# Kernel tuning notes

Hardware: AMD Instinct MI355X
Metric: run time of the kernel (lower is better)

## Reference

```python
import jax, jax.numpy as jnp
import numpy as np

H, D = 24, 128
HID = H * D  # 3072
IP_DIM = 2048
B, S_IMG, S_TXT, L_IP = 1, 1024, 512, 16
EPS = 1e-6
IP_SCALE = 1.0


def _rms(x, w):
    v = jnp.mean(jnp.square(x), axis=-1, keepdims=True)
    return x * jax.lax.rsqrt(v + EPS) * w


def _heads(x):
    b, s, _ = x.shape
    return x.reshape(b, s, H, D).transpose(0, 2, 1, 3)  # [b,H,s,D]


def _unheads(x):
    b, h, s, d = x.shape
    return x.transpose(0, 2, 1, 3).reshape(b, s, h * d)


def _rope(x, cos, sin):
    # diffusers flux apply_rotary_emb (use_real, unbind_dim=-1): interleaved pairs
    xr = x.reshape(x.shape[:-1] + (D // 2, 2))
    xrot = jnp.stack([-xr[..., 1], xr[..., 0]], axis=-1).reshape(x.shape)
    return x * cos + xrot * sin


def _sdpa(q, k, v):
    scale = 1.0 / jnp.sqrt(jnp.asarray(D, q.dtype))
    s = jnp.einsum('bhqd,bhkd->bhqk', q, k) * scale
    return jnp.einsum('bhqk,bhkd->bhqd', jax.nn.softmax(s, axis=-1), v)


def setup_inputs() -> dict:
    ks = iter(jax.random.split(jax.random.key(0), 24))
    std = 0.02
    lin = lambda k, di, do: std * jax.random.normal(k, (di, do), jnp.float32)
    z = lambda: jnp.zeros((HID,), jnp.float32)
    ones = lambda: jnp.ones((D,), jnp.float32)
    return {
        'hidden_states': jax.random.normal(next(ks), (B, S_IMG, HID), jnp.float32),
        'encoder_hidden_states': jax.random.normal(next(ks), (B, S_TXT, HID), jnp.float32),
        'ip_hidden_states': jax.random.normal(next(ks), (B, L_IP, IP_DIM), jnp.float32),
        'rope_cos': jax.random.uniform(next(ks), (S_TXT + S_IMG, D), jnp.float32),
        'rope_sin': jax.random.uniform(next(ks), (S_TXT + S_IMG, D), jnp.float32),
        'Wq': lin(next(ks), HID, HID), 'bq': z(),
        'Wk': lin(next(ks), HID, HID), 'bk': z(),
        'Wv': lin(next(ks), HID, HID), 'bv': z(),
        'norm_q_w': ones(), 'norm_k_w': ones(),
        'Waq': lin(next(ks), HID, HID), 'baq': z(),
        'Wak': lin(next(ks), HID, HID), 'bak': z(),
        'Wav': lin(next(ks), HID, HID), 'bav': z(),
        'norm_added_q_w': ones(), 'norm_added_k_w': ones(),
        'Wo': lin(next(ks), HID, HID), 'bo': z(),
        'Wadd_out': lin(next(ks), HID, HID), 'badd_out': z(),
        'Wk_ip': lin(next(ks), IP_DIM, HID), 'bk_ip': z(),
        'Wv_ip': lin(next(ks), IP_DIM, HID), 'bv_ip': z(),
        'norm_ip_q_w': ones(), 'norm_ip_k_w': ones(),
    }


def reference(hidden_states, encoder_hidden_states, ip_hidden_states, rope_cos, rope_sin,
              Wq, bq, Wk, bk, Wv, bv, norm_q_w, norm_k_w,
              Waq, baq, Wak, bak, Wav, bav, norm_added_q_w, norm_added_k_w,
              Wo, bo, Wadd_out, badd_out,
              Wk_ip, bk_ip, Wv_ip, bv_ip, norm_ip_q_w, norm_ip_k_w):
    s_txt = encoder_hidden_states.shape[1]
    # image-token projections
    q = hidden_states @ Wq + bq
    k = hidden_states @ Wk + bk
    v = hidden_states @ Wv + bv

    # IP-adapter cross-attention branch (uses q pre-RMSNorm / pre-RoPE)
    ip_q = _rms(_heads(q), norm_ip_q_w)                               # [B,H,S_img,D]
    ip_k = _rms(_heads(ip_hidden_states @ Wk_ip + bk_ip), norm_ip_k_w)  # [B,H,L_ip,D]
    ip_v = _heads(ip_hidden_states @ Wv_ip + bv_ip)
    ip_out = _unheads(_sdpa(ip_q, ip_k, ip_v))                        # [B,S_img,HID]

    qh = _rms(_heads(q), norm_q_w)
    kh = _rms(_heads(k), norm_k_w)
    vh = _heads(v)

    # text-token (encoder) projections
    eq = _rms(_heads(encoder_hidden_states @ Waq + baq), norm_added_q_w)
    ek = _rms(_heads(encoder_hidden_states @ Wak + bak), norm_added_k_w)
    ev = _heads(encoder_hidden_states @ Wav + bav)

    qf = _rope(jnp.concatenate([eq, qh], axis=2), rope_cos, rope_sin)
    kf = _rope(jnp.concatenate([ek, kh], axis=2), rope_cos, rope_sin)
    vf = jnp.concatenate([ev, vh], axis=2)

    out = _unheads(_sdpa(qf, kf, vf))                                 # [B,S_txt+S_img,HID]
    enc_out, img_out = out[:, :s_txt], out[:, s_txt:]
    img_out = img_out + ip_out * IP_SCALE
    img_out = img_out @ Wo + bo
    enc_out = enc_out @ Wadd_out + badd_out
    return (img_out, enc_out)
```

## Files before the change

kernel.cpp:

```cpp
#include <hip/hip_runtime.h>

typedef __bf16 bf16x8 __attribute__((ext_vector_type(8)));
typedef float f32x4 __attribute__((ext_vector_type(4)));
typedef unsigned short u16;
typedef unsigned int u32;

#define QSCALE 0.08838834764831845f

static __device__ __forceinline__ float bf2f(u16 u) {
  union { float f; u32 i; } x; x.i = ((u32)u) << 16; return x.f;
}
static __device__ __forceinline__ u16 f2bf(float f) {
  union { float f; u32 i; } x; x.f = f;
  u32 r = x.i + 0x7fffu + ((x.i >> 16) & 1u);
  return (u16)(r >> 16);
}
static __device__ __forceinline__ void gload16(const void* gp, void* lp) {
  __builtin_amdgcn_global_load_lds(
      (const __attribute__((address_space(1))) u32*)gp,
      (__attribute__((address_space(3))) u32*)lp, 16, 0, 0);
}

__global__ __launch_bounds__(256) void k_conv_acts(
    const float* __restrict__ hs, const float* __restrict__ ehs, const float* __restrict__ iph,
    u16* __restrict__ hsb, u16* __restrict__ ehsb, u16* __restrict__ ipb)
{
  int i = blockIdx.x * 256 + threadIdx.x;
  const float* s; u16* d; int j;
  if (i < 786432)        { s = hs;  d = hsb;  j = i; }
  else if (i < 1179648)  { s = ehs; d = ehsb; j = i - 786432; }
  else                   { s = iph; d = ipb;  j = i - 1179648; }
  float4 v = ((const float4*)s)[j];
  uint2 o;
  o.x = (u32)f2bf(v.x) | ((u32)f2bf(v.y) << 16);
  o.y = (u32)f2bf(v.z) | ((u32)f2bf(v.w) << 16);
  ((uint2*)d)[j] = o;
}

struct WT { const float* src; u16* dst; int K; };
struct WTPack { WT w[10]; };

__global__ __launch_bounds__(256) void k_transp_w(WTPack p)
{
  WT d = p.w[blockIdx.z];
  int K = d.K;
  int k0 = blockIdx.y * 64;
  if (k0 >= K) return;
  int n0 = blockIdx.x * 64;
  __shared__ u16 T[64 * 72];
  int tid = threadIdx.x;
  #pragma unroll
  for (int i = 0; i < 4; i++) {
    int idx = tid + i * 256;
    int r = idx >> 4, ch = idx & 15;
    float4 v = *(const float4*)(d.src + (size_t)(k0 + r) * 3072 + n0 + ch * 4);
    T[(ch*4+0)*72 + r] = f2bf(v.x);
    T[(ch*4+1)*72 + r] = f2bf(v.y);
    T[(ch*4+2)*72 + r] = f2bf(v.z);
    T[(ch*4+3)*72 + r] = f2bf(v.w);
  }
  __syncthreads();
  #pragma unroll
  for (int i = 0; i < 2; i++) {
    int idx = tid + i * 256;
    int r = idx >> 3, ch = idx & 7;
    uint4 v = *(const uint4*)(T + r * 72 + ch * 8);
    *(uint4*)(d.dst + (size_t)(n0 + r) * K + k0 + ch * 8) = v;
  }
}

struct GJob { const u16* A; const u16* W; const float* bias; void* C; int M; int K; int blk0; int out_f32; };
struct GPack { GJob j[8]; int njobs; };

__global__ __launch_bounds__(256) void k_gemm(GPack p)
{
  __shared__ u16 As[128 * 32];
  __shared__ u16 Bs[128 * 32];
  int bid = blockIdx.x;
  int ji = 0;
  while (ji + 1 < p.njobs && bid >= p.j[ji+1].blk0) ji++;
  GJob J = p.j[ji];
  int local = bid - J.blk0;
  int m0 = (local / 24) * 128;
  int n0 = (local % 24) * 128;

  int tid = threadIdx.x, w = tid >> 6, lane = tid & 63, l15 = lane & 15, quad = lane >> 4;
  int wm = (w >> 1) * 64, wn = (w & 1) * 64;
  f32x4 acc[4][4] = {};

  int s0 = tid, s1 = tid + 256;
  const u16* Ag0 = J.A + (size_t)(m0 + (s0 >> 2)) * J.K + (s0 & 3) * 8;
  const u16* Ag1 = J.A + (size_t)(m0 + (s1 >> 2)) * J.K + (s1 & 3) * 8;
  const u16* Bg0 = J.W + (size_t)(n0 + (s0 >> 2)) * J.K + (s0 & 3) * 8;
  const u16* Bg1 = J.W + (size_t)(n0 + (s1 >> 2)) * J.K + (s1 & 3) * 8;
  u16* lA0 = As + w * 512;
  u16* lA1 = As + 2048 + w * 512;
  u16* lB0 = Bs + w * 512;
  u16* lB1 = Bs + 2048 + w * 512;

  for (int k0 = 0; k0 < J.K; k0 += 32) {
    gload16(Ag0 + k0, lA0);
    gload16(Ag1 + k0, lA1);
    gload16(Bg0 + k0, lB0);
    gload16(Bg1 + k0, lB1);
    __syncthreads();
    bf16x8 af[4], bfr[4];
    #pragma unroll
    for (int t = 0; t < 4; t++) {
      af[t]  = *(const bf16x8*)(As + (wm + t * 16 + l15) * 32 + quad * 8);
      bfr[t] = *(const bf16x8*)(Bs + (wn + t * 16 + l15) * 32 + quad * 8);
    }
    #pragma unroll
    for (int mt = 0; mt < 4; mt++)
      #pragma unroll
      for (int nt = 0; nt < 4; nt++)
        acc[mt][nt] = __builtin_amdgcn_mfma_f32_16x16x32_bf16(af[mt], bfr[nt], acc[mt][nt], 0, 0, 0);
    __syncthreads();
  }

  #pragma unroll
  for (int mt = 0; mt < 4; mt++) {
    int row = m0 + wm + mt * 16 + quad * 4;
    #pragma unroll
    for (int nt = 0; nt < 4; nt++) {
      int col = n0 + wn + nt * 16 + l15;
      float bv = J.bias[col];
      #pragma unroll
      for (int r = 0; r < 4; r++) {
        if (row + r < J.M) {
          float v = acc[mt][nt][r] + bv;
          if (J.out_f32) ((float*)J.C)[(size_t)(row + r) * 3072 + col] = v;
          else           ((u16*)J.C)[(size_t)(row + r) * 3072 + col] = f2bf(v);
        }
      }
    }
  }
}

__global__ __launch_bounds__(256) void k_pack_qk(
    const u16* __restrict__ q, const u16* __restrict__ k,
    const u16* __restrict__ eq, const u16* __restrict__ ek,
    const u16* __restrict__ ipk,
    const float* __restrict__ cosr, const float* __restrict__ sinr,
    const float* __restrict__ nq, const float* __restrict__ nk,
    const float* __restrict__ naq, const float* __restrict__ nak,
    const float* __restrict__ nipq, const float* __restrict__ nipk,
    u16* __restrict__ Qf, u16* __restrict__ Kf, u16* __restrict__ Qip, u16* __restrict__ Kip)
{
  int u = blockIdx.x * 4 + (threadIdx.x >> 6);
  int lane = threadIdx.x & 63;
  int d0 = lane * 2;
  if (u < 36864) {
    int t = u / 24, h = u % 24;
    bool txt = t < 512;
    const u16* qrow = txt ? eq + (size_t)t * 3072 : q + (size_t)(t - 512) * 3072;
    const u16* krow = txt ? ek + (size_t)t * 3072 : k + (size_t)(t - 512) * 3072;
    u32 qv = ((const u32*)(qrow + h * 128))[lane];
    u32 kv = ((const u32*)(krow + h * 128))[lane];
    float q0 = bf2f((u16)qv), q1 = bf2f((u16)(qv >> 16));
    float k0 = bf2f((u16)kv), k1 = bf2f((u16)(kv >> 16));
    float sq = q0 * q0 + q1 * q1, sk = k0 * k0 + k1 * k1;
    #pragma unroll
    for (int off = 32; off > 0; off >>= 1) {
      sq += __shfl_xor(sq, off, 64);
      sk += __shfl_xor(sk, off, 64);
    }
    float rq = rsqrtf(sq * (1.0f / 128.0f) + 1e-6f);
    float rk = rsqrtf(sk * (1.0f / 128.0f) + 1e-6f);
    const float* wq = txt ? naq : nq;
    const float* wk = txt ? nak : nk;
    float2 c = ((const float2*)(cosr + (size_t)t * 128))[lane];
    float2 s = ((const float2*)(sinr + (size_t)t * 128))[lane];
    float xq0 = q0 * rq * wq[d0] * QSCALE, xq1 = q1 * rq * wq[d0 + 1] * QSCALE;
    float xk0 = k0 * rk * wk[d0],          xk1 = k1 * rk * wk[d0 + 1];
    u32 oq = (u32)f2bf(xq0 * c.x - xq1 * s.x) | ((u32)f2bf(xq1 * c.y + xq0 * s.y) << 16);
    u32 ok = (u32)f2bf(xk0 * c.x - xk1 * s.x) | ((u32)f2bf(xk1 * c.y + xk0 * s.y) << 16);
    ((u32*)(Qf + ((size_t)h * 1536 + t) * 128))[lane] = oq;
    ((u32*)(Kf + ((size_t)h * 1536 + t) * 128))[lane] = ok;
    if (!txt) {
      float y0 = q0 * rq * nipq[d0] * QSCALE, y1 = q1 * rq * nipq[d0 + 1] * QSCALE;
      u32 oy = (u32)f2bf(y0) | ((u32)f2bf(y1) << 16);
      ((u32*)(Qip + ((size_t)h * 1024 + (t - 512)) * 128))[lane] = oy;
    }
  } else {
    int u2 = u - 36864;
    if (u2 < 384) {
      int h = u2 >> 4, t = u2 & 15;
      u32 v = ((const u32*)(ipk + (size_t)t * 3072 + h * 128))[lane];
      float x0 = bf2f((u16)v), x1 = bf2f((u16)(v >> 16));
      float ss = x0 * x0 + x1 * x1;
      #pragma unroll
      for (int off = 32; off > 0; off >>= 1) ss += __shfl_xor(ss, off, 64);
      float rr = rsqrtf(ss * (1.0f / 128.0f) + 1e-6f);
      u32 o = (u32)f2bf(x0 * rr * nipk[d0]) | ((u32)f2bf(x1 * rr * nipk[d0 + 1]) << 16);
      ((u32*)(Kip + ((size_t)h * 64 + t) * 128))[lane] = o;
    }
  }
}

__global__ __launch_bounds__(256) void k_pack_v(
    const u16* __restrict__ v, const u16* __restrict__ ev, const u16* __restrict__ ipv,
    u16* __restrict__ Vt, u16* __restrict__ Vipt)
{
  __shared__ u16 T[64 * 72];
  int h = blockIdx.x, y = blockIdx.y, tid = threadIdx.x;
  if (y < 48) {
    int tb = (y % 24) * 64, db = (y / 24) * 64;
    #pragma unroll
    for (int i = 0; i < 2; i++) {
      int idx = tid + i * 256;
      int r = idx >> 3, ch = idx & 7;
      int t = tb + r;
      const u16* src = (t < 512) ? ev + (size_t)t * 3072 : v + (size_t)(t - 512) * 3072;
      uint4 val = *(const uint4*)(src + h * 128 + db + ch * 8);
      u16 tmp[8];
      *(uint4*)tmp = val;
      #pragma unroll
      for (int j = 0; j < 8; j++) T[(ch * 8 + j) * 72 + r] = tmp[j];
    }
    __syncthreads();
    #pragma unroll
    for (int i = 0; i < 2; i++) {
      int idx = tid + i * 256;
      int r = idx >> 3, ch = idx & 7;
      uint4 val = *(const uint4*)(T + r * 72 + ch * 8);
      *(uint4*)(Vt + ((size_t)h * 128 + db + r) * 1536 + tb + ch * 8) = val;
    }
  } else {
    if (tid < 128) {
      #pragma unroll
      for (int t = 0; t < 64; t++) {
        u16 val = 0;
        if (t < 16) val = ipv[(size_t)t * 3072 + h * 128 + tid];
        Vipt[((size_t)h * 128 + tid) * 64 + t] = val;
      }
    }
  }
}

__global__ __launch_bounds__(256) void k_attn(
    const u16* __restrict__ Q, const u16* __restrict__ K, const u16* __restrict__ V,
    const float* __restrict__ addend, void* __restrict__ out,
    int Sq, int Skv, int Skv_valid, int mode)
{
  __shared__ u16 Ks[64 * 128];
  __shared__ u16 Vs[128 * 64];
  __shared__ u16 Ps[4 * 16 * 68];
  int tid = threadIdx.x, h = blockIdx.y;
  int w = tid >> 6, lane = tid & 63, l15 = lane & 15, quad = lane >> 4;
  int mb = blockIdx.x * 64 + w * 16;

  bf16x8 aq[4];
  {
    const u16* qp = Q + ((size_t)h * Sq + mb + l15) * 128 + quad * 8;
    #pragma unroll
    for (int c = 0; c < 4; c++) aq[c] = *(const bf16x8*)(qp + c * 32);
  }

  const u16* Kg[4]; const u16* Vg[4];
  #pragma unroll
  for (int i = 0; i < 4; i++) {
    int s = tid + i * 256;
    int key = s >> 4, kc = (s & 15) ^ (key & 15);
    Kg[i] = K + ((size_t)h * Skv + key) * 128 + kc * 8;
    int d = s >> 3, vc = (s & 7) ^ (d & 7);
    Vg[i] = V + ((size_t)h * 128 + d) * Skv + vc * 8;
  }

  f32x4 o[8] = {};
  float m_col = -3.0e38f, l_col = 0.0f;
  u16* myPs = Ps + w * (16 * 68);

  for (int kb = 0; kb < Skv; kb += 64) {
    #pragma unroll
    for (int i = 0; i < 4; i++) {
      gload16(Kg[i] + (size_t)kb * 128, Ks + (i * 256 + w * 64) * 8);
      gload16(Vg[i] + kb,               Vs + (i * 256 + w * 64) * 8);
    }
    __syncthreads();

    f32x4 sc[4];
    #pragma unroll
    for (int mt = 0; mt < 4; mt++) {
      f32x4 a = {0.f, 0.f, 0.f, 0.f};
      int key = mt * 16 + l15;
      #pragma unroll
      for (int c = 0; c < 4; c++) {
        bf16x8 kf = *(const bf16x8*)(Ks + key * 128 + (((c * 4 + quad) ^ l15) * 8));
        a = __builtin_amdgcn_mfma_f32_16x16x32_bf16(kf, aq[c], a, 0, 0, 0);
      }
      sc[mt] = a;
    }
    if (Skv_valid != Skv) {
      #pragma unroll
      for (int mt = 0; mt < 4; mt++)
        #pragma unroll
        for (int r = 0; r < 4; r++)
          if (kb + mt * 16 + quad * 4 + r >= Skv_valid) sc[mt][r] = -1e30f;
    }

    float mx = sc[0][0];
    #pragma unroll
    for (int mt = 0; mt < 4; mt++)
      #pragma unroll
      for (int r = 0; r < 4; r++) mx = fmaxf(mx, sc[mt][r]);
    mx = fmaxf(mx, __shfl_xor(mx, 16, 64));
    mx = fmaxf(mx, __shfl_xor(mx, 32, 64));
    float mn = fmaxf(m_col, mx);
    float alpha = __expf(m_col - mn);
    m_col = mn;

    float sum = 0.f;
    #pragma unroll
    for (int mt = 0; mt < 4; mt++) {
      u16 pk[4];
      #pragma unroll
      for (int r = 0; r < 4; r++) {
        float pp = __expf(sc[mt][r] - mn);
        sum += pp;
        pk[r] = f2bf(pp);
      }
      uint2 pv;
      pv.x = (u32)pk[0] | ((u32)pk[1] << 16);
      pv.y = (u32)pk[2] | ((u32)pk[3] << 16);
      *(uint2*)(myPs + l15 * 68 + mt * 16 + quad * 4) = pv;
    }
    sum += __shfl_xor(sum, 16, 64);
    sum += __shfl_xor(sum, 32, 64);
    l_col = l_col * alpha + sum;

    float ar[4];
    #pragma unroll
    for (int r = 0; r < 4; r++) ar[r] = __shfl(alpha, quad * 4 + r, 64);
    #pragma unroll
    for (int nt = 0; nt < 8; nt++) {
      o[nt][0] *= ar[0]; o[nt][1] *= ar[1]; o[nt][2] *= ar[2]; o[nt][3] *= ar[3];
    }

    __asm__ volatile("s_waitcnt lgkmcnt(0)" ::: "memory");
    #pragma unroll
    for (int kc = 0; kc < 2; kc++) {
      bf16x8 pa = *(const bf16x8*)(myPs + l15 * 68 + kc * 32 + quad * 8);
      #pragma unroll
      for (int nt = 0; nt < 8; nt++) {
        int d = nt * 16 + l15;
        bf16x8 vf = *(const bf16x8*)(Vs + d * 64 + (((kc * 4 + quad) ^ (d & 7)) * 8));
        o[nt] = __builtin_amdgcn_mfma_f32_16x16x32_bf16(pa, vf, o[nt], 0, 0, 0);
      }
    }
    __syncthreads();
  }

  float linv = 1.0f / l_col;
  float lr[4];
  #pragma unroll
  for (int r = 0; r < 4; r++) lr[r] = __shfl(linv, quad * 4 + r, 64);
  #pragma unroll
  for (int r = 0; r < 4; r++) {
    int t = mb + quad * 4 + r;
    size_t base = (size_t)t * 3072 + h * 128 + l15;
    if (mode == 0) {
      float* O = (float*)out;
      #pragma unroll
      for (int nt = 0; nt < 8; nt++) O[base + nt * 16] = o[nt][r] * lr[r];
    } else {
      u16* O = (u16*)out;
      #pragma unroll
      for (int nt = 0; nt < 8; nt++) {
        float vv = o[nt][r] * lr[r];
        if (t >= 512) vv += addend[(size_t)(t - 512) * 3072 + h * 128 + nt * 16 + l15];
        O[base + nt * 16] = f2bf(vv);
      }
    }
  }
}

extern "C" void kernel_launch(void* const* d_in, const int* in_sizes, int n_in,
                              void* d_out, int out_size, void* d_ws, size_t ws_size,
                              hipStream_t stream) {
  const float* hs   = (const float*)d_in[0];
  const float* ehs  = (const float*)d_in[1];
  const float* iph  = (const float*)d_in[2];
  const float* cosr = (const float*)d_in[3];
  const float* sinr = (const float*)d_in[4];
  const float* Wq   = (const float*)d_in[5];  const float* bq   = (const float*)d_in[6];
  const float* Wk   = (const float*)d_in[7];  const float* bk   = (const float*)d_in[8];
  const float* Wv   = (const float*)d_in[9];  const float* bv   = (const float*)d_in[10];
  const float* nq   = (const float*)d_in[11]; const float* nk   = (const float*)d_in[12];
  const float* Waq  = (const float*)d_in[13]; const float* baq  = (const float*)d_in[14];
  const float* Wak  = (const float*)d_in[15]; const float* bak  = (const float*)d_in[16];
  const float* Wav  = (const float*)d_in[17]; const float* bav  = (const float*)d_in[18];
  const float* naq  = (const float*)d_in[19]; const float* nak  = (const float*)d_in[20];
  const float* Wo   = (const float*)d_in[21]; const float* bo   = (const float*)d_in[22];
  const float* Wad  = (const float*)d_in[23]; const float* bad  = (const float*)d_in[24];
  const float* Wkip = (const float*)d_in[25]; const float* bkip = (const float*)d_in[26];
  const float* Wvip = (const float*)d_in[27]; const float* bvip = (const float*)d_in[28];
  const float* nipq = (const float*)d_in[29]; const float* nipk = (const float*)d_in[30];
  (void)in_sizes; (void)n_in; (void)out_size; (void)ws_size;

  char* ws = (char*)d_ws;
  size_t off = 0;
  auto alloc = [&](size_t bytes) { size_t o = off; off += (bytes + 255) & ~(size_t)255; return o; };

  u16* hsb  = (u16*)(ws + alloc((size_t)1024 * 3072 * 2));
  u16* ehsb = (u16*)(ws + alloc((size_t)512 * 3072 * 2));
  u16* ipb  = (u16*)(ws + alloc((size_t)16 * 2048 * 2));
  u16* WT_[10];
  for (int i = 0; i < 10; i++) WT_[i] = (u16*)(ws + alloc((size_t)3072 * (i < 8 ? 3072 : 2048) * 2));
  u16* qb   = (u16*)(ws + alloc((size_t)1024 * 3072 * 2));
  u16* kb_  = (u16*)(ws + alloc((size_t)1024 * 3072 * 2));
  u16* vb   = (u16*)(ws + alloc((size_t)1024 * 3072 * 2));
  u16* eqb  = (u16*)(ws + alloc((size_t)512 * 3072 * 2));
  u16* ekb  = (u16*)(ws + alloc((size_t)512 * 3072 * 2));
  u16* evb  = (u16*)(ws + alloc((size_t)512 * 3072 * 2));
  u16* ipkb = (u16*)(ws + alloc((size_t)16 * 3072 * 2));
  u16* ipvb = (u16*)(ws + alloc((size_t)16 * 3072 * 2));
  u16* Qf   = (u16*)(ws + alloc((size_t)24 * 1536 * 128 * 2));
  u16* Kff  = (u16*)(ws + alloc((size_t)24 * 1536 * 128 * 2));
  u16* Vt   = (u16*)(ws + alloc((size_t)24 * 128 * 1536 * 2));
  u16* Qip  = (u16*)(ws + alloc((size_t)24 * 1024 * 128 * 2));
  u16* Kip  = (u16*)(ws + alloc((size_t)24 * 64 * 128 * 2));
  u16* Vipt = (u16*)(ws + alloc((size_t)24 * 128 * 64 * 2));
  float* ip_out = (float*)(ws + alloc((size_t)1024 * 3072 * 4));
  u16* attnb = (u16*)(ws + alloc((size_t)1536 * 3072 * 2));

  k_conv_acts<<<4640, 256, 0, stream>>>(hs, ehs, iph, hsb, ehsb, ipb);

  WTPack p;
  const float* wsrc[10] = {Wq, Wk, Wv, Waq, Wak, Wav, Wo, Wad, Wkip, Wvip};
  for (int i = 0; i < 10; i++) { p.w[i].src = wsrc[i]; p.w[i].dst = WT_[i]; p.w[i].K = (i < 8 ? 3072 : 2048); }
  k_transp_w<<<dim3(48, 48, 10), 256, 0, stream>>>(p);

  {
    GPack pp;
    const u16* As_[8]  = {hsb, hsb, hsb, ehsb, ehsb, ehsb, ipb, ipb};
    const u16* Ws_[8]  = {WT_[0], WT_[1], WT_[2], WT_[3], WT_[4], WT_[5], WT_[8], WT_[9]};
    const float* bs_[8] = {bq, bk, bv, baq, bak, bav, bkip, bvip};
    u16* Cs_[8]        = {qb, kb_, vb, eqb, ekb, evb, ipkb, ipvb};
    int Ms_[8] = {1024, 1024, 1024, 512, 512, 512, 16, 16};
    int Ks_[8] = {3072, 3072, 3072, 3072, 3072, 3072, 2048, 2048};
    int blk = 0;
    for (int i = 0; i < 8; i++) {
      pp.j[i].A = As_[i]; pp.j[i].W = Ws_[i]; pp.j[i].bias = bs_[i]; pp.j[i].C = Cs_[i];
      pp.j[i].M = Ms_[i]; pp.j[i].K = Ks_[i]; pp.j[i].blk0 = blk; pp.j[i].out_f32 = 0;
      blk += ((Ms_[i] + 127) / 128) * 24;
    }
    pp.njobs = 8;
    k_gemm<<<dim3(blk), 256, 0, stream>>>(pp);
  }

  k_pack_qk<<<9312, 256, 0, stream>>>(qb, kb_, eqb, ekb, ipkb, cosr, sinr, nq, nk, naq, nak, nipq, nipk, Qf, Kff, Qip, Kip);
  k_pack_v<<<dim3(24, 49), 256, 0, stream>>>(vb, evb, ipvb, Vt, Vipt);

  k_attn<<<dim3(16, 24), 256, 0, stream>>>(Qip, Kip, Vipt, (const float*)nullptr, ip_out, 1024, 64, 16, 0);
  k_attn<<<dim3(24, 24), 256, 0, stream>>>(Qf, Kff, Vt, ip_out, attnb, 1536, 1536, 1536, 1);

  {
    GPack pp;
    float* out = (float*)d_out;
    pp.j[0].A = attnb + (size_t)512 * 3072; pp.j[0].W = WT_[6]; pp.j[0].bias = bo;
    pp.j[0].C = out; pp.j[0].M = 1024; pp.j[0].K = 3072; pp.j[0].blk0 = 0; pp.j[0].out_f32 = 1;
    pp.j[1].A = attnb; pp.j[1].W = WT_[7]; pp.j[1].bias = bad;
    pp.j[1].C = out + (size_t)1024 * 3072; pp.j[1].M = 512; pp.j[1].K = 3072; pp.j[1].blk0 = 192; pp.j[1].out_f32 = 1;
    pp.njobs = 2;
    k_gemm<<<dim3(288), 256, 0, stream>>>(pp);
  }
}
```

Before: 786.3 us.

## Deepen GEMM K-tile to 64 with XOR-swizzled LDS and templated M-tile

The GEMM kernel now loads 64-wide K slices per iteration instead of 32, which halves the number of barrier pairs per tile. LDS rows are XOR-swizzled to avoid bank conflicts on the wider rows. The M tile becomes a template parameter: the output projections use 64-row tiles to double the block count (576 vs 288) for better CU occupancy. The trade-off is more LDS per block and, for the 64-row variant, less reuse per loaded B tile.

Result: faster. 728.5 us (-7.4%).

```diff
diff --git a/kernel.cpp b/kernel.cpp
--- a/kernel.cpp
+++ b/kernel.cpp
@@ -72,54 +72,68 @@
 struct GJob { const u16* A; const u16* W; const float* bias; void* C; int M; int K; int blk0; int out_f32; };
 struct GPack { GJob j[8]; int njobs; };
 
+template<int MT>
 __global__ __launch_bounds__(256) void k_gemm(GPack p)
 {
-  __shared__ u16 As[128 * 32];
-  __shared__ u16 Bs[128 * 32];
+  __shared__ u16 As[MT * 64];
+  __shared__ u16 Bs[128 * 64];
   int bid = blockIdx.x;
   int ji = 0;
   while (ji + 1 < p.njobs && bid >= p.j[ji+1].blk0) ji++;
   GJob J = p.j[ji];
   int local = bid - J.blk0;
-  int m0 = (local / 24) * 128;
+  int m0 = (local / 24) * MT;
   int n0 = (local % 24) * 128;
 
   int tid = threadIdx.x, w = tid >> 6, lane = tid & 63, l15 = lane & 15, quad = lane >> 4;
-  int wm = (w >> 1) * 64, wn = (w & 1) * 64;
-  f32x4 acc[4][4] = {};
-
-  int s0 = tid, s1 = tid + 256;
-  const u16* Ag0 = J.A + (size_t)(m0 + (s0 >> 2)) * J.K + (s0 & 3) * 8;
-  const u16* Ag1 = J.A + (size_t)(m0 + (s1 >> 2)) * J.K + (s1 & 3) * 8;
-  const u16* Bg0 = J.W + (size_t)(n0 + (s0 >> 2)) * J.K + (s0 & 3) * 8;
-  const u16* Bg1 = J.W + (size_t)(n0 + (s1 >> 2)) * J.K + (s1 & 3) * 8;
-  u16* lA0 = As + w * 512;
-  u16* lA1 = As + 2048 + w * 512;
-  u16* lB0 = Bs + w * 512;
-  u16* lB1 = Bs + 2048 + w * 512;
-
-  for (int k0 = 0; k0 < J.K; k0 += 32) {
-    gload16(Ag0 + k0, lA0);
-    gload16(Ag1 + k0, lA1);
-    gload16(Bg0 + k0, lB0);
-    gload16(Bg1 + k0, lB1);
+  constexpr int MF = MT / 32;
+  int wm = (w >> 1) * (MT / 2), wn = (w & 1) * 64;
+  f32x4 acc[MF][4] = {};
+
+  constexpr int GA = MT * 8 / 256;
+  const u16* Ag[GA]; const u16* Bg[4];
+  #pragma unroll
+  for (int i = 0; i < GA; i++) {
+    int s = i * 256 + tid;
+    int row = s >> 3, kc = (s & 7) ^ (row & 7);
+    Ag[i] = J.A + (size_t)(m0 + row) * J.K + kc * 8;
+  }
+  #pragma unroll
+  for (int i = 0; i < 4; i++) {
+    int s = i * 256 + tid;
+    int row = s >> 3, kc = (s & 7) ^ (row & 7);
+    Bg[i] = J.W + (size_t)(n0 + row) * J.K + kc * 8;
+  }
+
+  for (int k0 = 0; k0 < J.K; k0 += 64) {
+    #pragma unroll
+    for (int i = 0; i < GA; i++)
+      gload16(Ag[i] + k0, As + (size_t)(i * 256 + w * 64) * 8);
+    #pragma unroll
+    for (int i = 0; i < 4; i++)
+      gload16(Bg[i] + k0, Bs + (size_t)(i * 256 + w * 64) * 8);
     __syncthreads();
-    bf16x8 af[4], bfr[4];
-    #pragma unroll
-    for (int t = 0; t < 4; t++) {
-      af[t]  = *(const bf16x8*)(As + (wm + t * 16 + l15) * 32 + quad * 8);
-      bfr[t] = *(const bf16x8*)(Bs + (wn + t * 16 + l15) * 32 + quad * 8);
-    }
-    #pragma unroll
-    for (int mt = 0; mt < 4; mt++)
-      #pragma unroll
-      for (int nt = 0; nt < 4; nt++)
-        acc[mt][nt] = __builtin_amdgcn_mfma_f32_16x16x32_bf16(af[mt], bfr[nt], acc[mt][nt], 0, 0, 0);
+    int x7 = l15 & 7;
+    #pragma unroll
+    for (int ks = 0; ks < 2; ks++) {
+      bf16x8 af[MF], bfr[4];
+      #pragma unroll
+      for (int t = 0; t < MF; t++)
+        af[t] = *(const bf16x8*)(As + (wm + t * 16 + l15) * 64 + (((ks * 4 + quad) ^ x7) * 8));
+      #pragma unroll
+      for (int t = 0; t < 4; t++)
+        bfr[t] = *(const bf16x8*)(Bs + (wn + t * 16 + l15) * 64 + (((ks * 4 + quad) ^ x7) * 8));
+      #pragma unroll
+      for (int mt = 0; mt < MF; mt++)
+        #pragma unroll
+        for (int nt = 0; nt < 4; nt++)
+          acc[mt][nt] = __builtin_amdgcn_mfma_f32_16x16x32_bf16(af[mt], bfr[nt], acc[mt][nt], 0, 0, 0);
+    }
     __syncthreads();
   }
 
   #pragma unroll
-  for (int mt = 0; mt < 4; mt++) {
+  for (int mt = 0; mt < MF; mt++) {
     int row = m0 + wm + mt * 16 + quad * 4;
     #pragma unroll
     for (int nt = 0; nt < 4; nt++) {
@@ -446,7 +460,7 @@
       blk += ((Ms_[i] + 127) / 128) * 24;
     }
     pp.njobs = 8;
-    k_gemm<<<dim3(blk), 256, 0, stream>>>(pp);
+    k_gemm<128><<<dim3(blk), 256, 0, stream>>>(pp);
   }
 
   k_pack_qk<<<9312, 256, 0, stream>>>(qb, kb_, eqb, ekb, ipkb, cosr, sinr, nq, nk, naq, nak, nipq, nipk, Qf, Kff, Qip, Kip);
@@ -461,8 +475,9 @@
     pp.j[0].A = attnb + (size_t)512 * 3072; pp.j[0].W = WT_[6]; pp.j[0].bias = bo;
     pp.j[0].C = out; pp.j[0].M = 1024; pp.j[0].K = 3072; pp.j[0].blk0 = 0; pp.j[0].out_f32 = 1;
     pp.j[1].A = attnb; pp.j[1].W = WT_[7]; pp.j[1].bias = bad;
-    pp.j[1].C = out + (size_t)1024 * 3072; pp.j[1].M = 512; pp.j[1].K = 3072; pp.j[1].blk0 = 192; pp.j[1].out_f32 = 1;
+    pp.j[1].C = out + (size_t)1024 * 3072; pp.j[1].M = 512; pp.j[1].K = 3072;
+    pp.j[1].blk0 = (1024 / 64) * 24; pp.j[1].out_f32 = 1;
     pp.njobs = 2;
-    k_gemm<<<dim3(288), 256, 0, stream>>>(pp);
-  }
-}
+    k_gemm<64><<<dim3((1024 / 64) * 24 + (512 / 64) * 24), 256, 0, stream>>>(pp);
+  }
+}
```
